# Performance work log

Measured on AMD Instinct MI355X. Metric: run time of the kernel, lower is better.

## Reference

```python
import jax, jax.numpy as jnp
import numpy as np

N_FFT = 1024
HOP = 256
WIN = 1024
SIG_LEN = 16777216  # 2**24 samples


def _hamming_sym(M):
    # scipy.signal.hamming(M, sym=True): 0.54 - 0.46*cos(2*pi*n/(M-1))
    n = np.arange(M)
    return (0.54 - 0.46 * np.cos(2.0 * np.pi * n / (M - 1))).astype(np.float32)


def setup_inputs() -> dict:
    key = jax.random.key(0)
    x = jax.random.normal(key, (SIG_LEN,), dtype=jnp.float32)
    return {"x": x}


def reference(x):
    # window, normalized by sqrt(n_fft) (sum of Hamming window is nonzero)
    win = jnp.asarray(_hamming_sym(WIN) / np.sqrt(N_FFT).astype(np.float32))
    hw2 = WIN // 2
    half_n = N_FFT // 2 + 1
    pad = 3 * HOP

    xp = jnp.pad(x, (pad, pad))       # np.append zeros on both sides
    total = xp.shape[0]
    n_rows = total // HOP             # allocated output rows (trailing rows stay zero)
    n_frames = (total - WIN) // HOP + 1  # frames actually computed by the while-loop

    starts = jnp.arange(n_frames) * HOP
    frames = xp[starts[:, None] + jnp.arange(WIN)[None, :]] * win

    # zero-phase buffer: buf[:hw1] = win_x[hw2:], buf[-hw2:] = win_x[:hw2]
    mid = jnp.zeros((n_frames, N_FFT - WIN), dtype=frames.dtype)
    buf = jnp.concatenate([frames[:, hw2:], mid, frames[:, :hw2]], axis=1)

    spec = jnp.fft.rfft(buf, n=N_FFT, axis=1)        # [n_frames, half_n] complex64
    mag = jnp.abs(spec).astype(jnp.float32)
    ph = jnp.angle(spec).astype(jnp.float32)

    xm_x = jnp.zeros((n_rows, half_n), jnp.float32).at[:n_frames].set(mag)
    xp_x = jnp.zeros((n_rows, half_n), jnp.float32).at[:n_frames].set(ph)
    return (xm_x, xp_x)
```

## Files before the change

### kernel.cpp

```cpp
#include <hip/hip_runtime.h>


#define SIG_LEN   16777216
#define N_FRAMES  65539
#define N_ROWS    65542
#define HALF_N    513
#define FRAMES_FLOATS (N_FRAMES * HALF_N)
#define MAG_SZ        (N_ROWS   * HALF_N)


__global__ void init_tables(double* __restrict__ ws) {
  int i = blockIdx.x * 256 + threadIdx.x;
  const double PI = 3.14159265358979323846;
  if (i < 1024) {
    ws[i] = (0.54 - 0.46 * cos(2.0 * PI * (double)i / 1023.0)) / 32.0;
  }
  if (i < 448) {
    int l = i / 7, r = i % 7 + 1;
    double a = -2.0 * PI * (double)(l * r) / 512.0;
    ws[1024 + 2 * i]     = cos(a);
    ws[1024 + 2 * i + 1] = sin(a);
  }
  if (i < 56) {
    int q = i / 7, r = i % 7 + 1;
    double a = -2.0 * PI * (double)(8 * q * r) / 512.0;
    ws[1920 + 2 * i]     = cos(a);
    ws[1920 + 2 * i + 1] = sin(a);
  }
  if (i < 513) {
    double th = PI * (double)i / 512.0;
    double c = cos(th), s = sin(th);
    ws[2048 + 4 * i]     = 0.5 * (1.0 - s);
    ws[2048 + 4 * i + 1] = -0.5 * c;
    ws[2048 + 4 * i + 2] = 0.5 * (1.0 + s);
    ws[2048 + 4 * i + 3] = 0.5 * c;
  }
}

__global__ void zero_tail(float* __restrict__ out) {
  int i = blockIdx.x * 256 + threadIdx.x;
  if (i < (MAG_SZ - FRAMES_FLOATS)) {
    out[FRAMES_FLOATS + i] = 0.0f;
    out[MAG_SZ + FRAMES_FLOATS + i] = 0.0f;
  }
}

#define CMUL(vr, vi, wx, wy) { double _t = (vr)*(wx) - (vi)*(wy); \
                               (vi) = (vr)*(wy) + (vi)*(wx); (vr) = _t; }

__device__ __forceinline__ void dft8(double* ar, double* ai) {
  const double S = 0.70710678118654752440;
  double s0r = ar[0] + ar[4], s0i = ai[0] + ai[4];
  double s1r = ar[0] - ar[4], s1i = ai[0] - ai[4];
  double s2r = ar[2] + ar[6], s2i = ai[2] + ai[6];
  double s3r = ar[2] - ar[6], s3i = ai[2] - ai[6];
  double t0r = ar[1] + ar[5], t0i = ai[1] + ai[5];
  double t1r = ar[1] - ar[5], t1i = ai[1] - ai[5];
  double t2r = ar[3] + ar[7], t2i = ai[3] + ai[7];
  double t3r = ar[3] - ar[7], t3i = ai[3] - ai[7];

  double e0r = s0r + s2r, e0i = s0i + s2i;
  double e2r = s0r - s2r, e2i = s0i - s2i;
  double e1r = s1r + s3i, e1i = s1i - s3r;
  double e3r = s1r - s3i, e3i = s1i + s3r;
  double o0r = t0r + t2r, o0i = t0i + t2i;
  double o2r = t0r - t2r, o2i = t0i - t2i;
  double o1r = t1r + t3i, o1i = t1i - t3r;
  double o3r = t1r - t3i, o3i = t1i + t3r;

  double u1r = S * (o1r + o1i), u1i = S * (o1i - o1r);
  double u2r = o2i,             u2i = -o2r;
  double u3r = S * (o3i - o3r), u3i = -S * (o3r + o3i);

  ar[0] = e0r + o0r; ai[0] = e0i + o0i;
  ar[4] = e0r - o0r; ai[4] = e0i - o0i;
  ar[1] = e1r + u1r; ai[1] = e1i + u1i;
  ar[5] = e1r - u1r; ai[5] = e1i - u1i;
  ar[2] = e2r + u2r; ai[2] = e2i + u2i;
  ar[6] = e2r - u2r; ai[6] = e2i - u2i;
  ar[3] = e3r + u3r; ai[3] = e3i + u3i;
  ar[7] = e3r - u3r; ai[7] = e3i - u3i;
}

__global__ __launch_bounds__(256, 5) void stft_frame(const float* __restrict__ x,
                                                     const double* __restrict__ ws,
                                                     float* __restrict__ out) {
  __shared__ double2 zbuf[4][512];

  const int wv = threadIdx.x >> 6;
  const int l  = threadIdx.x & 63;
  const int f  = blockIdx.x * 4 + wv;
  if (f >= N_FRAMES) return;
  double2* z = zbuf[wv];

  const int g = l >> 3;
  const int q = l & 7;

  double ar[8], ai[8];
  const int base = f * 256 - 768;
  if (base >= 0 && base + 1024 <= SIG_LEN) {
#pragma unroll
    for (int n2 = 0; n2 < 8; ++n2) {
      int j = 128 * n2 + 2 * l;
      float2 xv = *(const float2*)(x + base + j);
      double2 wn = *(const double2*)(ws + j);
      ar[n2] = (double)xv.x * wn.x;
      ai[n2] = (double)xv.y * wn.y;
    }
  } else {
#pragma unroll
    for (int n2 = 0; n2 < 8; ++n2) {
      int j  = 128 * n2 + 2 * l;
      int ix = base + j;
      double v0 = (ix >= 0 && ix < SIG_LEN) ? (double)x[ix] : 0.0;
      double v1 = (ix + 1 >= 0 && ix + 1 < SIG_LEN) ? (double)x[ix + 1] : 0.0;
      double2 wn = *(const double2*)(ws + j);
      ar[n2] = v0 * wn.x;
      ai[n2] = v1 * wn.y;
    }
  }

  dft8(ar, ai);
  {
    const double2* tw1 = (const double2*)(ws + 1024) + l * 7;
#pragma unroll
    for (int r = 1; r < 8; ++r) {
      double2 w = tw1[r - 1];
      CMUL(ar[r], ai[r], w.x, w.y);
    }
  }

#pragma unroll
  for (int r = 0; r < 8; ++r) {
    z[64 * r + 8 * g + (q ^ g)] = make_double2(ar[r], ai[r]);
  }
  asm volatile("s_waitcnt lgkmcnt(0)" ::: "memory");
#pragma unroll
  for (int r = 0; r < 8; ++r) {
    double2 v = z[64 * g + 8 * r + (q ^ r)];
    ar[r] = v.x; ai[r] = v.y;
  }

  dft8(ar, ai);
  {
    const double2* tw2 = (const double2*)(ws + 1920) + q * 7;
#pragma unroll
    for (int r = 1; r < 8; ++r) {
      double2 w = tw2[r - 1];
      CMUL(ar[r], ai[r], w.x, w.y);
    }
  }

#pragma unroll
  for (int r = 0; r < 8; ++r) {
    z[64 * g + 8 * r + (q ^ r)] = make_double2(ar[r], ai[r]);
  }
  asm volatile("s_waitcnt lgkmcnt(0)" ::: "memory");
#pragma unroll
  for (int r = 0; r < 8; ++r) {
    double2 v = z[64 * g + 8 * q + (r ^ q)];
    ar[r] = v.x; ai[r] = v.y;
  }

  dft8(ar, ai);

#pragma unroll
  for (int r = 0; r < 8; ++r) {
    z[64 * r + 8 * q + (g ^ q)] = make_double2(ar[r], ai[r]);
  }
  asm volatile("s_waitcnt lgkmcnt(0)" ::: "memory");

  const double* AB = ws + 2048;
  const int czk = 8 * (l >> 3) + ((l & 7) ^ (l >> 3));
  const float sgn = (l & 1) ? -1.0f : 1.0f;
#pragma unroll
  for (int i = 0; i < 8; ++i) {
    int k = l + 64 * i;
    double2 Zk = z[64 * i + czk];
    int km = (512 - k) & 511;
    double2 Zm = z[(km & ~7) | ((km ^ (km >> 3)) & 7)];
    const double* ab = AB + 4 * k;
    double Axv = ab[0], Ayv = ab[1], Bxv = ab[2], Byv = ab[3];
    double Yr = Zk.x * Axv - Zk.y * Ayv + Zm.x * Bxv + Zm.y * Byv;
    double Yi = Zk.x * Ayv + Zk.y * Axv + Zm.x * Byv - Zm.y * Bxv;
    if (i == 0 && l == 0) Yi = 0.0;
    float yr = (float)Yr;
    float yi = (float)Yi;
    float mag = sqrtf(yr * yr + yi * yi);
    float ph = atan2f(sgn * yi, sgn * yr);
    out[f * HALF_N + k] = mag;
    out[MAG_SZ + f * HALF_N + k] = ph;
  }

  if (l == 0) {
    double2 z0 = z[0];
    double Yr = z0.x - z0.y;
    float yr = (float)Yr;
    out[f * HALF_N + 512] = fabsf(yr);
    out[MAG_SZ + f * HALF_N + 512] =
        __builtin_signbitf(yr) ? 3.14159265358979323846f : 0.0f;
  }
}

extern "C" void kernel_launch(void* const* d_in, const int* in_sizes, int n_in,
                              void* d_out, int out_size, void* d_ws, size_t ws_size,
                              hipStream_t stream) {
  const float* x = (const float*)d_in[0];
  float* out = (float*)d_out;
  double* ws = (double*)d_ws;

  hipLaunchKernelGGL(init_tables, dim3(4), dim3(256), 0, stream, ws);
  hipLaunchKernelGGL(zero_tail, dim3(7), dim3(256), 0, stream, out);
  hipLaunchKernelGGL(stft_frame, dim3((N_FRAMES + 3) / 4), dim3(256), 0, stream,
                     x, ws, out);
}
```

Baseline: 403.5 us.

## Exploit conjugate symmetry in post-processing, use fast atan2/sqrt, shrink blocks

Each lane now computes bins k and 512-k together from the same pair of loaded Z values. This halves the post-processing loop iterations and shared-memory reads, and the Nyquist/center bins are handled separately. The libm atan2f and sqrtf are replaced by a polynomial atan2 approximation built on the hardware reciprocal, plus the raw hardware sqrt, at some cost in accuracy. Blocks shrink from four wavefronts to two, which changes occupancy and scheduling granularity.

```diff
diff --git a/kernel.cpp b/kernel.cpp
--- a/kernel.cpp
+++ b/kernel.cpp
@@ -82,14 +82,33 @@
   ar[7] = e3r - u3r; ai[7] = e3i - u3i;
 }
 
-__global__ __launch_bounds__(256, 5) void stft_frame(const float* __restrict__ x,
+__device__ __forceinline__ float fast_atan2f(float y, float x) {
+  const float PI   = 3.14159265358979f;
+  const float PI_2 = 1.57079632679490f;
+  float ax = fabsf(x), ay = fabsf(y);
+  float mx = fmaxf(ax, ay), mn = fminf(ax, ay);
+  float t = mn * __builtin_amdgcn_rcpf(mx);
+  t = (mx == 0.0f) ? 0.0f : t;
+  float zz = t * t;
+  float a = fmaf(zz, -0.01172120f, 0.05265332f);
+  a = fmaf(zz, a, -0.11643287f);
+  a = fmaf(zz, a,  0.19354346f);
+  a = fmaf(zz, a, -0.33262347f);
+  a = fmaf(zz, a,  0.99997726f);
+  a = a * t;
+  a = (ay > ax) ? (PI_2 - a) : a;
+  a = (x < 0.0f) ? (PI - a) : a;
+  return copysignf(a, y);
+}
+
+__global__ __launch_bounds__(128, 5) void stft_frame(const float* __restrict__ x,
                                                      const double* __restrict__ ws,
                                                      float* __restrict__ out) {
-  __shared__ double2 zbuf[4][512];
+  __shared__ double2 zbuf[2][512];
 
   const int wv = threadIdx.x >> 6;
   const int l  = threadIdx.x & 63;
-  const int f  = blockIdx.x * 4 + wv;
+  const int f  = blockIdx.x * 2 + wv;
   if (f >= N_FRAMES) return;
   double2* z = zbuf[wv];
 
@@ -171,34 +190,44 @@
   asm volatile("s_waitcnt lgkmcnt(0)" ::: "memory");
 
   const double* AB = ws + 2048;
-  const int czk = 8 * (l >> 3) + ((l & 7) ^ (l >> 3));
+  const int czk = 8 * g + (q ^ g);
   const float sgn = (l & 1) ? -1.0f : 1.0f;
-#pragma unroll
-  for (int i = 0; i < 8; ++i) {
-    int k = l + 64 * i;
+  float* outm = out + f * HALF_N;
+  float* outp = out + MAG_SZ + f * HALF_N;
+#pragma unroll
+  for (int i = 0; i < 4; ++i) {
+    int k  = 64 * i + l;
+    int km = 512 - k;
     double2 Zk = z[64 * i + czk];
-    int km = (512 - k) & 511;
-    double2 Zm = z[(km & ~7) | ((km ^ (km >> 3)) & 7)];
+    int zmi = km & 511;
+    zmi = (zmi & ~7) | ((zmi ^ (zmi >> 3)) & 7);
+    double2 Zm = z[zmi];
     const double* ab = AB + 4 * k;
     double Axv = ab[0], Ayv = ab[1], Bxv = ab[2], Byv = ab[3];
-    double Yr = Zk.x * Axv - Zk.y * Ayv + Zm.x * Bxv + Zm.y * Byv;
-    double Yi = Zk.x * Ayv + Zk.y * Axv + Zm.x * Byv - Zm.y * Bxv;
-    if (i == 0 && l == 0) Yi = 0.0;
-    float yr = (float)Yr;
-    float yi = (float)Yi;
-    float mag = sqrtf(yr * yr + yi * yi);
-    float ph = atan2f(sgn * yi, sgn * yr);
-    out[f * HALF_N + k] = mag;
-    out[MAG_SZ + f * HALF_N + k] = ph;
+    double Yr  = Zk.x * Axv - Zk.y * Ayv + Zm.x * Bxv + Zm.y * Byv;
+    double Yi  = Zk.x * Ayv + Zk.y * Axv + Zm.x * Byv - Zm.y * Bxv;
+    double Y2r = Zm.x * Axv + Zm.y * Ayv + Zk.x * Bxv - Zk.y * Byv;
+    double Y2i = -(Zm.x * Ayv - Zm.y * Axv + Zk.x * Byv + Zk.y * Bxv);
+    if (i == 0) {
+      if (l == 0) { Yi = 0.0; Y2i = 0.0; }
+    }
+    float yr  = (float)Yr,  yi  = (float)Yi;
+    float y2r = (float)Y2r, y2i = (float)Y2i;
+    float mag1 = __builtin_amdgcn_sqrtf(fmaf(yr, yr, yi * yi));
+    float ph1  = fast_atan2f(sgn * yi, sgn * yr);
+    float mag2 = __builtin_amdgcn_sqrtf(fmaf(y2r, y2r, y2i * y2i));
+    float ph2  = fast_atan2f(sgn * y2i, sgn * y2r);
+    outm[k]  = mag1;
+    outp[k]  = ph1;
+    outm[km] = mag2;
+    outp[km] = ph2;
   }
 
   if (l == 0) {
-    double2 z0 = z[0];
-    double Yr = z0.x - z0.y;
-    float yr = (float)Yr;
-    out[f * HALF_N + 512] = fabsf(yr);
-    out[MAG_SZ + f * HALF_N + 512] =
-        __builtin_signbitf(yr) ? 3.14159265358979323846f : 0.0f;
+    double2 zc = z[256];
+    float yr = (float)zc.x, yi = (float)(-zc.y);
+    outm[256] = __builtin_amdgcn_sqrtf(fmaf(yr, yr, yi * yi));
+    outp[256] = fast_atan2f(yi, yr);
   }
 }
 
@@ -211,6 +240,6 @@
 
   hipLaunchKernelGGL(init_tables, dim3(4), dim3(256), 0, stream, ws);
   hipLaunchKernelGGL(zero_tail, dim3(7), dim3(256), 0, stream, out);
-  hipLaunchKernelGGL(stft_frame, dim3((N_FRAMES + 3) / 4), dim3(256), 0, stream,
+  hipLaunchKernelGGL(stft_frame, dim3((N_FRAMES + 1) / 2), dim3(128), 0, stream,
                      x, ws, out);
 }
```

Measured after the change: 400.1 us. No clear change (-0.9%).
